# Performance work log

Hardware: AMD Instinct MI355X
Metric: run time of the kernel (lower is better)

The kernel has to match this reference:

```python
import jax, jax.numpy as jnp
import numpy as np
import math

B, LQ, LK = 2, 2048, 2048
DIM = 1024
H = 16
DH = DIM // H


def setup_inputs() -> dict:
    key = jax.random.key(0)
    ks = jax.random.split(key, 12)
    s = 1.0 / math.sqrt(DIM)
    return {
        "query": jax.random.normal(ks[0], (B, LQ, DIM), jnp.float32),
        "key": jax.random.normal(ks[1], (B, LK, DIM), jnp.float32),
        "value": jax.random.normal(ks[2], (B, LK, DIM), jnp.float32),
        "mask": jnp.zeros((B, LQ, LK), dtype=bool),
        "Wq": jax.random.normal(ks[3], (DIM, DIM), jnp.float32) * s,
        "bq": jax.random.normal(ks[4], (DIM,), jnp.float32) * s,
        "Wk": jax.random.normal(ks[5], (DIM, DIM), jnp.float32) * s,
        "bk": jax.random.normal(ks[6], (DIM,), jnp.float32) * s,
        "Wv": jax.random.normal(ks[7], (DIM, DIM), jnp.float32) * s,
        "bv": jax.random.normal(ks[8], (DIM,), jnp.float32) * s,
        "Wo": jax.random.normal(ks[9], (DIM, DIM), jnp.float32) * s,
        "bo": jax.random.normal(ks[10], (DIM,), jnp.float32) * s,
    }


def reference(query, key, value, mask, Wq, bq, Wk, bk, Wv, bv, Wo, bo):
    b = query.shape[0]

    def shape(x):  # (b, l, dim) -> (b, h, l, dh)
        return x.reshape(b, -1, H, DH).transpose(0, 2, 1, 3)

    q = shape(query @ Wq.T + bq)
    k = shape(key @ Wk.T + bk)
    v = shape(value @ Wv.T + bv)

    q = q / math.sqrt(DH)
    # (b, h, lq, lk) score matrix, computed in float32 as the original does
    scores = jnp.einsum("bhqd,bhkd->bhqk", q, k).astype(jnp.float32)
    scores = jnp.where(mask[:, None, :, :], jnp.float32(-1e18), scores)
    attn = jax.nn.softmax(scores, axis=-1).astype(q.dtype)
    context = jnp.einsum("bhqk,bhkd->bhqd", attn, v)
    context = context.transpose(0, 2, 1, 3).reshape(b, -1, H * DH)
    return context @ Wo.T + bo
```

## Files before the change

kernel.cpp:

```cpp
#include <hip/hip_runtime.h>
#include <hip/hip_bf16.h>

typedef __attribute__((ext_vector_type(4))) float float4v;
typedef __attribute__((ext_vector_type(8))) __bf16 bf16x8;
typedef __attribute__((ext_vector_type(4))) unsigned short ushort4v;

#define MFMA16(a, b, c) __builtin_amdgcn_mfma_f32_16x16x32_bf16(a, b, c, 0, 0, 0)

__device__ __forceinline__ unsigned short f2bf(float f) {
    return __builtin_bit_cast(unsigned short, (__bf16)f);
}

__device__ __forceinline__ float fast_exp2(float x) {
#if __has_builtin(__builtin_amdgcn_exp2f)
    return __builtin_amdgcn_exp2f(x);
#else
    return exp2f(x);
#endif
}

__device__ __forceinline__ void gl_lds16(const unsigned short* g, unsigned short* l) {
    __builtin_amdgcn_global_load_lds(
        (const __attribute__((address_space(1))) void*)g,
        (__attribute__((address_space(3))) void*)l, 16, 0, 0);
}

struct CvtSeg { const float* s; unsigned short* d; int n; };
struct Cvt7 { CvtSeg seg[7]; };

__global__ __launch_bounds__(256) void cvt_kernel(Cvt7 a) {
    const CvtSeg c = a.seg[blockIdx.y];
    const int stride = gridDim.x * 256 * 4;
    for (int i = (blockIdx.x * 256 + threadIdx.x) * 4; i < c.n; i += stride) {
        float4v v = *(const float4v*)(c.s + i);
        ushort4v u;
        u.x = f2bf(v.x); u.y = f2bf(v.y); u.z = f2bf(v.z); u.w = f2bf(v.w);
        *(ushort4v*)(c.d + i) = u;
    }
}

__device__ __forceinline__ void gemm128_body(const unsigned short* __restrict__ A,
                                             const unsigned short* __restrict__ W,
                                             const float* __restrict__ bias,
                                             unsigned short* __restrict__ Cout,
                                             int N, int K, float scale,
                                             unsigned short* As, unsigned short* Ws) {
    const int t = threadIdx.x;
    const int w = t >> 6, lane = t & 63;
    const int quad = lane >> 4, l16 = lane & 15;
    const int m0 = blockIdx.x * 128, n0 = blockIdx.y * 128;
    const int wm = (w >> 1) * 64, wn = (w & 1) * 64;

    float4v acc[4][4];
    for (int i = 0; i < 4; ++i)
        for (int j = 0; j < 4; ++j) acc[i][j] = float4v{0.f, 0.f, 0.f, 0.f};

    const int srow = lane >> 3;
    const int scol = (lane & 7) * 8;

    for (int k0 = 0; k0 < K; k0 += 64) {
        __syncthreads();
        for (int i = 0; i < 4; ++i) {
            const int c = w * 4 + i;
            gl_lds16(A + (size_t)(m0 + c * 8 + srow) * K + k0 + scol,
                     &As[c * 512 + lane * 8]);
            gl_lds16(W + (size_t)(n0 + c * 8 + srow) * K + k0 + scol,
                     &Ws[c * 512 + lane * 8]);
        }
        __syncthreads();
        for (int ks = 0; ks < 2; ++ks) {
            bf16x8 af[4], wf[4];
            for (int i = 0; i < 4; ++i)
                af[i] = *(const bf16x8*)&As[(wm + i * 16 + l16) * 64 + ks * 32 + quad * 8];
            for (int i = 0; i < 4; ++i)
                wf[i] = *(const bf16x8*)&Ws[(wn + i * 16 + l16) * 64 + ks * 32 + quad * 8];
            for (int mi = 0; mi < 4; ++mi)
                for (int ni = 0; ni < 4; ++ni)
                    acc[mi][ni] = MFMA16(af[mi], wf[ni], acc[mi][ni]);
        }
    }

    for (int mi = 0; mi < 4; ++mi)
        for (int ni = 0; ni < 4; ++ni) {
            const int col = n0 + wn + ni * 16 + l16;
            const float bv = bias[col];
            for (int reg = 0; reg < 4; ++reg) {
                const int row = m0 + wm + mi * 16 + quad * 4 + reg;
                Cout[(size_t)row * N + col] = f2bf((acc[mi][ni][reg] + bv) * scale);
            }
        }
}

__global__ __launch_bounds__(256) void gemm_qkv_kernel(
    const unsigned short* qa, const unsigned short* ka, const unsigned short* va,
    const unsigned short* Wqb, const unsigned short* Wkb, const unsigned short* Wvb,
    const float* bq, const float* bk, const float* bv,
    unsigned short* Qb, unsigned short* Kb, unsigned short* Vb, float qscale) {
    __shared__ unsigned short As[128 * 64];
    __shared__ unsigned short Ws[128 * 64];
    const int z = blockIdx.z;
    const unsigned short* A = z == 0 ? qa : (z == 1 ? ka : va);
    const unsigned short* W = z == 0 ? Wqb : (z == 1 ? Wkb : Wvb);
    const float* bias = z == 0 ? bq : (z == 1 ? bk : bv);
    unsigned short* C = z == 0 ? Qb : (z == 1 ? Kb : Vb);
    gemm128_body(A, W, bias, C, 1024, 1024, z == 0 ? qscale : 1.0f, As, Ws);
}

__global__ __launch_bounds__(256) void gemm_out_kernel(const unsigned short* __restrict__ A,
                                                       const unsigned short* __restrict__ W,
                                                       const float* __restrict__ bias,
                                                       float* __restrict__ Cout) {
    __shared__ unsigned short As[64 * 64];
    __shared__ unsigned short Ws[128 * 64];
    const int N = 1024, K = 1024;
    const int t = threadIdx.x;
    const int w = t >> 6, lane = t & 63;
    const int quad = lane >> 4, l16 = lane & 15;
    const int m0 = blockIdx.x * 64, n0 = blockIdx.y * 128;
    const int wm = (w & 1) * 32, wn = (w >> 1) * 64;

    float4v acc[2][4];
    for (int i = 0; i < 2; ++i)
        for (int j = 0; j < 4; ++j) acc[i][j] = float4v{0.f, 0.f, 0.f, 0.f};

    const int srow = lane >> 3;
    const int scol = (lane & 7) * 8;

    for (int k0 = 0; k0 < K; k0 += 64) {
        __syncthreads();
        for (int i = 0; i < 2; ++i) {
            const int c = w * 2 + i;
            gl_lds16(A + (size_t)(m0 + c * 8 + srow) * K + k0 + scol,
                     &As[c * 512 + lane * 8]);
        }
        for (int i = 0; i < 4; ++i) {
            const int c = w * 4 + i;
            gl_lds16(W + (size_t)(n0 + c * 8 + srow) * K + k0 + scol,
                     &Ws[c * 512 + lane * 8]);
        }
        __syncthreads();
        for (int ks = 0; ks < 2; ++ks) {
            bf16x8 af[2], wf[4];
            for (int i = 0; i < 2; ++i)
                af[i] = *(const bf16x8*)&As[(wm + i * 16 + l16) * 64 + ks * 32 + quad * 8];
            for (int i = 0; i < 4; ++i)
                wf[i] = *(const bf16x8*)&Ws[(wn + i * 16 + l16) * 64 + ks * 32 + quad * 8];
            for (int mi = 0; mi < 2; ++mi)
                for (int ni = 0; ni < 4; ++ni)
                    acc[mi][ni] = MFMA16(af[mi], wf[ni], acc[mi][ni]);
        }
    }

    for (int mi = 0; mi < 2; ++mi)
        for (int ni = 0; ni < 4; ++ni) {
            const int col = n0 + wn + ni * 16 + l16;
            const float bv = bias[col];
            for (int reg = 0; reg < 4; ++reg) {
                const int row = m0 + wm + mi * 16 + quad * 4 + reg;
                Cout[(size_t)row * N + col] = acc[mi][ni][reg] + bv;
            }
        }
}

__global__ __launch_bounds__(256) void attn_kernel(const unsigned short* __restrict__ Q,
                                                   const unsigned short* __restrict__ Kg,
                                                   const unsigned short* __restrict__ Vg,
                                                   const unsigned char* __restrict__ mask,
                                                   unsigned short* __restrict__ Ctx) {
    const int bid = blockIdx.x;
    const int bh = bid & 31;
    const int qt = bid >> 5;
    const int b = bh >> 4, h = bh & 15;
    const int t = threadIdx.x, w = t >> 6, lane = t & 63;
    const int quad = lane >> 4, l16 = lane & 15;

    __shared__ unsigned short Pt[128][72];
    __shared__ unsigned short Ks[64][72];
    __shared__ unsigned short Vt[64][72];

    const unsigned short* Qp = Q + ((size_t)(b * 2048 + qt * 128)) * 1024 + h * 64;
    const unsigned short* Kp = Kg + ((size_t)b * 2048) * 1024 + h * 64;
    const unsigned short* Vp = Vg + ((size_t)b * 2048) * 1024 + h * 64;
    const unsigned char* Mp = mask + (size_t)(b * 2048 + qt * 128) * 2048;

    for (int p = 0; p < 4; ++p) {
        const int idx = t + p * 256;
        const int r = idx >> 3, c8 = (idx & 7) * 8;
        *(uint4*)&Pt[r][c8] = *(const uint4*)(Qp + (size_t)r * 1024 + c8);
    }
    __syncthreads();
    bf16x8 qf[2][2];
    for (int c = 0; c < 2; ++c)
        for (int ks = 0; ks < 2; ++ks)
            qf[c][ks] = *(const bf16x8*)&Pt[w * 32 + c * 16 + l16][ks * 32 + quad * 8];

    float4v o[2][4];
    for (int c = 0; c < 2; ++c)
        for (int i = 0; i < 4; ++i) o[c][i] = float4v{0.f, 0.f, 0.f, 0.f};
    float l_acc[2] = {0.f, 0.f};

    const int sr = t >> 3, sc8 = (t & 7) * 8;
    const int vkk = (t & 31) * 2, vd0 = (t >> 5) * 8;
    const int mrow = w * 32 + (lane >> 1);
    const int mc0 = (lane & 1) * 32;

    uint4 kreg0, kreg1, vreg0, vreg1, mreg0, mreg1;
    {
        kreg0 = *(const uint4*)(Kp + (size_t)sr * 1024 + sc8);
        kreg1 = *(const uint4*)(Kp + (size_t)(sr + 32) * 1024 + sc8);
        vreg0 = *(const uint4*)(Vp + (size_t)vkk * 1024 + vd0);
        vreg1 = *(const uint4*)(Vp + (size_t)(vkk + 1) * 1024 + vd0);
        mreg0 = *(const uint4*)(Mp + (size_t)mrow * 2048 + mc0);
        mreg1 = *(const uint4*)(Mp + (size_t)mrow * 2048 + mc0 + 16);
    }

    for (int kc = 0; kc < 2048; kc += 64) {
        __syncthreads();
        *(uint4*)&Ks[sr][sc8] = kreg0;
        *(uint4*)&Ks[sr + 32][sc8] = kreg1;
        {
            const unsigned short* pa = (const unsigned short*)&vreg0;
            const unsigned short* pb = (const unsigned short*)&vreg1;
            for (int j = 0; j < 8; ++j)
                *(unsigned int*)&Vt[vd0 + j][vkk] =
                    (unsigned int)pa[j] | ((unsigned int)pb[j] << 16);
        }
        const unsigned int mor = mreg0.x | mreg0.y | mreg0.z | mreg0.w |
                                 mreg1.x | mreg1.y | mreg1.z | mreg1.w;
        const bool anymask = __any(mor != 0);
        __syncthreads();

        const int kn = kc + 64;
        if (kn < 2048) {
            kreg0 = *(const uint4*)(Kp + (size_t)(kn + sr) * 1024 + sc8);
            kreg1 = *(const uint4*)(Kp + (size_t)(kn + sr + 32) * 1024 + sc8);
            vreg0 = *(const uint4*)(Vp + (size_t)(kn + vkk) * 1024 + vd0);
            vreg1 = *(const uint4*)(Vp + (size_t)(kn + vkk + 1) * 1024 + vd0);
            mreg0 = *(const uint4*)(Mp + (size_t)mrow * 2048 + kn + mc0);
            mreg1 = *(const uint4*)(Mp + (size_t)mrow * 2048 + kn + mc0 + 16);
        }

        float4v s0[4], s1[4];
        for (int nt = 0; nt < 4; ++nt) {
            const float4v z4 = float4v{0.f, 0.f, 0.f, 0.f};
            bf16x8 kf = *(const bf16x8*)&Ks[nt * 16 + l16][quad * 8];
            s0[nt] = MFMA16(kf, qf[0][0], z4);
            s1[nt] = MFMA16(kf, qf[1][0], z4);
            kf = *(const bf16x8*)&Ks[nt * 16 + l16][32 + quad * 8];
            s0[nt] = MFMA16(kf, qf[0][1], s0[nt]);
            s1[nt] = MFMA16(kf, qf[1][1], s1[nt]);
        }

        for (int c = 0; c < 2; ++c) {
            float4v* s = c ? s1 : s0;
            const int qrow = w * 32 + c * 16 + l16;
            float lc = l_acc[c];
            for (int nt = 0; nt < 4; ++nt) {
                float p0 = s[nt][0], p1 = s[nt][1], p2 = s[nt][2], p3 = s[nt][3];
                if (anymask) {
                    const unsigned char* mr =
                        Mp + (size_t)qrow * 2048 + kc + nt * 16 + quad * 4;
                    if (mr[0]) p0 = -1e18f;
                    if (mr[1]) p1 = -1e18f;
                    if (mr[2]) p2 = -1e18f;
                    if (mr[3]) p3 = -1e18f;
                }
                const float e0 = fast_exp2(p0), e1 = fast_exp2(p1);
                const float e2 = fast_exp2(p2), e3 = fast_exp2(p3);
                lc += (e0 + e1) + (e2 + e3);
                uint2 u;
                u.x = (unsigned int)f2bf(e0) | ((unsigned int)f2bf(e1) << 16);
                u.y = (unsigned int)f2bf(e2) | ((unsigned int)f2bf(e3) << 16);
                *(uint2*)&Pt[qrow][nt * 16 + quad * 4] = u;
            }
            l_acc[c] = lc;
        }

        for (int ks = 0; ks < 2; ++ks) {
            bf16x8 pf0 = *(const bf16x8*)&Pt[w * 32 + l16][ks * 32 + quad * 8];
            bf16x8 pf1 = *(const bf16x8*)&Pt[w * 32 + 16 + l16][ks * 32 + quad * 8];
            for (int dt = 0; dt < 4; ++dt) {
                bf16x8 vf = *(const bf16x8*)&Vt[dt * 16 + l16][ks * 32 + quad * 8];
                o[0][dt] = MFMA16(pf0, vf, o[0][dt]);
                o[1][dt] = MFMA16(pf1, vf, o[1][dt]);
            }
        }
    }

    float lfull[2];
    for (int c = 0; c < 2; ++c) {
        float l = l_acc[c];
        l += __shfl_xor(l, 16);
        l += __shfl_xor(l, 32);
        lfull[c] = l;
    }

    for (int c = 0; c < 2; ++c) {
        float inv[4];
        for (int reg = 0; reg < 4; ++reg)
            inv[reg] = 1.0f / __shfl(lfull[c], (lane & 48) | (quad * 4 + reg));
        for (int dt = 0; dt < 4; ++dt) {
            const int dcol = dt * 16 + l16;
            for (int reg = 0; reg < 4; ++reg) {
                const int ql = w * 32 + c * 16 + quad * 4 + reg;
                Ctx[((size_t)(b * 2048 + qt * 128 + ql)) * 1024 + h * 64 + dcol] =
                    f2bf(o[c][dt][reg] * inv[reg]);
            }
        }
    }
}

extern "C" void kernel_launch(void* const* d_in, const int* in_sizes, int n_in,
                              void* d_out, int out_size, void* d_ws, size_t ws_size,
                              hipStream_t stream) {
    (void)in_sizes; (void)n_in; (void)out_size; (void)ws_size;
    const float* query = (const float*)d_in[0];
    const float* key   = (const float*)d_in[1];
    const float* value = (const float*)d_in[2];
    const unsigned char* mask = (const unsigned char*)d_in[3];
    const float* Wq = (const float*)d_in[4];
    const float* bq = (const float*)d_in[5];
    const float* Wk = (const float*)d_in[6];
    const float* bk = (const float*)d_in[7];
    const float* Wv = (const float*)d_in[8];
    const float* bv = (const float*)d_in[9];
    const float* Wo = (const float*)d_in[10];
    const float* bo = (const float*)d_in[11];

    const size_t MD = (size_t)4096 * 1024;
    const size_t WD = (size_t)1024 * 1024;

    unsigned short* Qb  = (unsigned short*)d_ws;
    unsigned short* Kb  = Qb + MD;
    unsigned short* Vb  = Kb + MD;
    unsigned short* qb  = Vb + MD;
    unsigned short* kb  = qb + MD;
    unsigned short* vb  = kb + MD;
    unsigned short* Wqb = vb + MD;
    unsigned short* Wkb = Wqb + WD;
    unsigned short* Wvb = Wkb + WD;
    unsigned short* Wob = Wvb + WD;
    unsigned short* Cb  = qb;

    Cvt7 cv;
    cv.seg[0] = {query, qb, (int)MD};
    cv.seg[1] = {key,   kb, (int)MD};
    cv.seg[2] = {value, vb, (int)MD};
    cv.seg[3] = {Wq, Wqb, (int)WD};
    cv.seg[4] = {Wk, Wkb, (int)WD};
    cv.seg[5] = {Wv, Wvb, (int)WD};
    cv.seg[6] = {Wo, Wob, (int)WD};
    cvt_kernel<<<dim3(1024, 7), 256, 0, stream>>>(cv);

    const float qscale = 0.125f * 1.44269504088896f;
    gemm_qkv_kernel<<<dim3(32, 8, 3), 256, 0, stream>>>(
        qb, kb, vb, Wqb, Wkb, Wvb, bq, bk, bv, Qb, Kb, Vb, qscale);

    attn_kernel<<<dim3(512), 256, 0, stream>>>(Qb, Kb, Vb, mask, Cb);

    gemm_out_kernel<<<dim3(64, 8), 256, 0, stream>>>(Cb, Wob, bo, (float*)d_out);
}
```

Measured before the change: 267.8 us.

## Fuse activation fp32-to-bf16 conversion into QKV GEMM and emit transposed V

The QKV projection GEMM now reads the fp32 query/key/value activations directly and packs them to bf16 while staging into shared memory, so the separate conversion pass over the activations is removed and only the weights are still converted. The V projection writes its output transposed (head-dim major) via a shared-memory staging tile, which lets the attention kernel load V with plain vector stores instead of a scalar transpose into LDS. The intent is to cut a large global read/write round trip and the LDS transpose cost. In exchange, the A-tile load now goes through registers rather than async global-to-LDS copies, and the V epilogue adds a sync and a strided write pattern.

Result: slower. 287.0 us (+7.2%).

```diff
diff --git a/kernel.cpp b/kernel.cpp
--- a/kernel.cpp
+++ b/kernel.cpp
@@ -25,10 +25,19 @@
         (__attribute__((address_space(3))) void*)l, 16, 0, 0);
 }
 
+__device__ __forceinline__ uint4 pack8bf(float4v a0, float4v a1) {
+    uint4 u;
+    u.x = (unsigned int)f2bf(a0.x) | ((unsigned int)f2bf(a0.y) << 16);
+    u.y = (unsigned int)f2bf(a0.z) | ((unsigned int)f2bf(a0.w) << 16);
+    u.z = (unsigned int)f2bf(a1.x) | ((unsigned int)f2bf(a1.y) << 16);
+    u.w = (unsigned int)f2bf(a1.z) | ((unsigned int)f2bf(a1.w) << 16);
+    return u;
+}
+
 struct CvtSeg { const float* s; unsigned short* d; int n; };
-struct Cvt7 { CvtSeg seg[7]; };
-
-__global__ __launch_bounds__(256) void cvt_kernel(Cvt7 a) {
+struct Cvt4 { CvtSeg seg[4]; };
+
+__global__ __launch_bounds__(256) void cvt_kernel(Cvt4 a) {
     const CvtSeg c = a.seg[blockIdx.y];
     const int stride = gridDim.x * 256 * 4;
     for (int i = (blockIdx.x * 256 + threadIdx.x) * 4; i < c.n; i += stride) {
@@ -39,12 +48,22 @@
     }
 }
 
-__device__ __forceinline__ void gemm128_body(const unsigned short* __restrict__ A,
-                                             const unsigned short* __restrict__ W,
-                                             const float* __restrict__ bias,
-                                             unsigned short* __restrict__ Cout,
-                                             int N, int K, float scale,
-                                             unsigned short* As, unsigned short* Ws) {
+__global__ __launch_bounds__(256) void gemm_qkv_kernel(
+    const float* qa, const float* ka, const float* va,
+    const unsigned short* Wqb, const unsigned short* Wkb, const unsigned short* Wvb,
+    const float* bq, const float* bk, const float* bv,
+    unsigned short* Qb, unsigned short* Kb, unsigned short* Vtg, float qscale) {
+    __shared__ unsigned short Sm[17408];
+    unsigned short* As = Sm;
+    unsigned short* Ws = Sm + 8192;
+
+    const int z = blockIdx.z;
+    const float* A = z == 0 ? qa : (z == 1 ? ka : va);
+    const unsigned short* W = z == 0 ? Wqb : (z == 1 ? Wkb : Wvb);
+    const float* bias = z == 0 ? bq : (z == 1 ? bk : bv);
+    const float scale = z == 0 ? qscale : 1.0f;
+
+    const int K = 1024, N = 1024;
     const int t = threadIdx.x;
     const int w = t >> 6, lane = t & 63;
     const int quad = lane >> 4, l16 = lane & 15;
@@ -55,15 +74,20 @@
     for (int i = 0; i < 4; ++i)
         for (int j = 0; j < 4; ++j) acc[i][j] = float4v{0.f, 0.f, 0.f, 0.f};
 
-    const int srow = lane >> 3;
-    const int scol = (lane & 7) * 8;
+    const int arow = t >> 3, acol = (t & 7) * 8;
+    const int srow = lane >> 3, scol = (lane & 7) * 8;
 
     for (int k0 = 0; k0 < K; k0 += 64) {
         __syncthreads();
+        for (int p = 0; p < 4; ++p) {
+            const int r = arow + p * 32;
+            const float* ap = A + (size_t)(m0 + r) * K + k0 + acol;
+            float4v a0 = *(const float4v*)ap;
+            float4v a1 = *(const float4v*)(ap + 4);
+            *(uint4*)&As[r * 64 + acol] = pack8bf(a0, a1);
+        }
         for (int i = 0; i < 4; ++i) {
             const int c = w * 4 + i;
-            gl_lds16(A + (size_t)(m0 + c * 8 + srow) * K + k0 + scol,
-                     &As[c * 512 + lane * 8]);
             gl_lds16(W + (size_t)(n0 + c * 8 + srow) * K + k0 + scol,
                      &Ws[c * 512 + lane * 8]);
         }
@@ -80,30 +104,35 @@
         }
     }
 
-    for (int mi = 0; mi < 4; ++mi)
-        for (int ni = 0; ni < 4; ++ni) {
-            const int col = n0 + wn + ni * 16 + l16;
-            const float bv = bias[col];
-            for (int reg = 0; reg < 4; ++reg) {
-                const int row = m0 + wm + mi * 16 + quad * 4 + reg;
-                Cout[(size_t)row * N + col] = f2bf((acc[mi][ni][reg] + bv) * scale);
-            }
-        }
-}
-
-__global__ __launch_bounds__(256) void gemm_qkv_kernel(
-    const unsigned short* qa, const unsigned short* ka, const unsigned short* va,
-    const unsigned short* Wqb, const unsigned short* Wkb, const unsigned short* Wvb,
-    const float* bq, const float* bk, const float* bv,
-    unsigned short* Qb, unsigned short* Kb, unsigned short* Vb, float qscale) {
-    __shared__ unsigned short As[128 * 64];
-    __shared__ unsigned short Ws[128 * 64];
-    const int z = blockIdx.z;
-    const unsigned short* A = z == 0 ? qa : (z == 1 ? ka : va);
-    const unsigned short* W = z == 0 ? Wqb : (z == 1 ? Wkb : Wvb);
-    const float* bias = z == 0 ? bq : (z == 1 ? bk : bv);
-    unsigned short* C = z == 0 ? Qb : (z == 1 ? Kb : Vb);
-    gemm128_body(A, W, bias, C, 1024, 1024, z == 0 ? qscale : 1.0f, As, Ws);
+    if (z < 2) {
+        unsigned short* C = z == 0 ? Qb : Kb;
+        for (int mi = 0; mi < 4; ++mi)
+            for (int ni = 0; ni < 4; ++ni) {
+                const int col = n0 + wn + ni * 16 + l16;
+                const float bvv = bias[col];
+                for (int reg = 0; reg < 4; ++reg) {
+                    const int row = m0 + wm + mi * 16 + quad * 4 + reg;
+                    C[(size_t)row * N + col] = f2bf((acc[mi][ni][reg] + bvv) * scale);
+                }
+            }
+    } else {
+        __syncthreads();
+        for (int mi = 0; mi < 4; ++mi)
+            for (int ni = 0; ni < 4; ++ni) {
+                const int col = wn + ni * 16 + l16;
+                const float bvv = bias[n0 + col];
+                for (int reg = 0; reg < 4; ++reg) {
+                    const int row = wm + mi * 16 + quad * 4 + reg;
+                    Sm[col * 136 + row] = f2bf(acc[mi][ni][reg] + bvv);
+                }
+            }
+        __syncthreads();
+        const int col = t >> 1, rb = (t & 1) * 64;
+        for (int j = 0; j < 8; ++j) {
+            uint4 v = *(const uint4*)&Sm[col * 136 + rb + j * 8];
+            *(uint4*)&Vtg[(size_t)(n0 + col) * 4096 + m0 + rb + j * 8] = v;
+        }
+    }
 }
 
 __global__ __launch_bounds__(256) void gemm_out_kernel(const unsigned short* __restrict__ A,
@@ -164,7 +193,7 @@
 
 __global__ __launch_bounds__(256) void attn_kernel(const unsigned short* __restrict__ Q,
                                                    const unsigned short* __restrict__ Kg,
-                                                   const unsigned short* __restrict__ Vg,
+                                                   const unsigned short* __restrict__ Vtg,
                                                    const unsigned char* __restrict__ mask,
                                                    unsigned short* __restrict__ Ctx) {
     const int bid = blockIdx.x;
@@ -180,7 +209,7 @@
 
     const unsigned short* Qp = Q + ((size_t)(b * 2048 + qt * 128)) * 1024 + h * 64;
     const unsigned short* Kp = Kg + ((size_t)b * 2048) * 1024 + h * 64;
-    const unsigned short* Vp = Vg + ((size_t)b * 2048) * 1024 + h * 64;
+    const unsigned short* Vp = Vtg + (size_t)(h * 64) * 4096 + b * 2048;
     const unsigned char* Mp = mask + (size_t)(b * 2048 + qt * 128) * 2048;
 
     for (int p = 0; p < 4; ++p) {
@@ -200,7 +229,7 @@
     float l_acc[2] = {0.f, 0.f};
 
     const int sr = t >> 3, sc8 = (t & 7) * 8;
-    const int vkk = (t & 31) * 2, vd0 = (t >> 5) * 8;
+    const int vd = t >> 2, vs0 = (t & 3) * 16;
     const int mrow = w * 32 + (lane >> 1);
     const int mc0 = (lane & 1) * 32;
 
@@ -208,8 +237,8 @@
     {
         kreg0 = *(const uint4*)(Kp + (size_t)sr * 1024 + sc8);
         kreg1 = *(const uint4*)(Kp + (size_t)(sr + 32) * 1024 + sc8);
-        vreg0 = *(const uint4*)(Vp + (size_t)vkk * 1024 + vd0);
-        vreg1 = *(const uint4*)(Vp + (size_t)(vkk + 1) * 1024 + vd0);
+        vreg0 = *(const uint4*)(Vp + (size_t)vd * 4096 + vs0);
+        vreg1 = *(const uint4*)(Vp + (size_t)vd * 4096 + vs0 + 8);
         mreg0 = *(const uint4*)(Mp + (size_t)mrow * 2048 + mc0);
         mreg1 = *(const uint4*)(Mp + (size_t)mrow * 2048 + mc0 + 16);
     }
@@ -218,13 +247,8 @@
         __syncthreads();
         *(uint4*)&Ks[sr][sc8] = kreg0;
         *(uint4*)&Ks[sr + 32][sc8] = kreg1;
-        {
-            const unsigned short* pa = (const unsigned short*)&vreg0;
-            const unsigned short* pb = (const unsigned short*)&vreg1;
-            for (int j = 0; j < 8; ++j)
-                *(unsigned int*)&Vt[vd0 + j][vkk] =
-                    (unsigned int)pa[j] | ((unsigned int)pb[j] << 16);
-        }
+        *(uint4*)&Vt[vd][vs0] = vreg0;
+        *(uint4*)&Vt[vd][vs0 + 8] = vreg1;
         const unsigned int mor = mreg0.x | mreg0.y | mreg0.z | mreg0.w |
                                  mreg1.x | mreg1.y | mreg1.z | mreg1.w;
         const bool anymask = __any(mor != 0);
@@ -234,8 +258,8 @@
         if (kn < 2048) {
             kreg0 = *(const uint4*)(Kp + (size_t)(kn + sr) * 1024 + sc8);
             kreg1 = *(const uint4*)(Kp + (size_t)(kn + sr + 32) * 1024 + sc8);
-            vreg0 = *(const uint4*)(Vp + (size_t)(kn + vkk) * 1024 + vd0);
-            vreg1 = *(const uint4*)(Vp + (size_t)(kn + vkk + 1) * 1024 + vd0);
+            vreg0 = *(const uint4*)(Vp + (size_t)vd * 4096 + kn + vs0);
+            vreg1 = *(const uint4*)(Vp + (size_t)vd * 4096 + kn + vs0 + 8);
             mreg0 = *(const uint4*)(Mp + (size_t)mrow * 2048 + kn + mc0);
             mreg1 = *(const uint4*)(Mp + (size_t)mrow * 2048 + kn + mc0 + 16);
         }
@@ -332,31 +356,25 @@
 
     unsigned short* Qb  = (unsigned short*)d_ws;
     unsigned short* Kb  = Qb + MD;
-    unsigned short* Vb  = Kb + MD;
-    unsigned short* qb  = Vb + MD;
-    unsigned short* kb  = qb + MD;
-    unsigned short* vb  = kb + MD;
-    unsigned short* Wqb = vb + MD;
+    unsigned short* Vtg = Kb + MD;
+    unsigned short* Wqb = Vtg + MD;
     unsigned short* Wkb = Wqb + WD;
     unsigned short* Wvb = Wkb + WD;
     unsigned short* Wob = Wvb + WD;
-    unsigned short* Cb  = qb;
-
-    Cvt7 cv;
-    cv.seg[0] = {query, qb, (int)MD};
-    cv.seg[1] = {key,   kb, (int)MD};
-    cv.seg[2] = {value, vb, (int)MD};
-    cv.seg[3] = {Wq, Wqb, (int)WD};
-    cv.seg[4] = {Wk, Wkb, (int)WD};
-    cv.seg[5] = {Wv, Wvb, (int)WD};
-    cv.seg[6] = {Wo, Wob, (int)WD};
-    cvt_kernel<<<dim3(1024, 7), 256, 0, stream>>>(cv);
+    unsigned short* Cb  = Wob + WD;
+
+    Cvt4 cv;
+    cv.seg[0] = {Wq, Wqb, (int)WD};
+    cv.seg[1] = {Wk, Wkb, (int)WD};
+    cv.seg[2] = {Wv, Wvb, (int)WD};
+    cv.seg[3] = {Wo, Wob, (int)WD};
+    cvt_kernel<<<dim3(256, 4), 256, 0, stream>>>(cv);
 
     const float qscale = 0.125f * 1.44269504088896f;
     gemm_qkv_kernel<<<dim3(32, 8, 3), 256, 0, stream>>>(
-        qb, kb, vb, Wqb, Wkb, Wvb, bq, bk, bv, Qb, Kb, Vb, qscale);
-
-    attn_kernel<<<dim3(512), 256, 0, stream>>>(Qb, Kb, Vb, mask, Cb);
+        query, key, value, Wqb, Wkb, Wvb, bq, bk, bv, Qb, Kb, Vtg, qscale);
+
+    attn_kernel<<<dim3(512), 256, 0, stream>>>(Qb, Kb, Vtg, mask, Cb);
 
     gemm_out_kernel<<<dim3(64, 8), 256, 0, stream>>>(Cb, Wob, bo, (float*)d_out);
 }
```
